# Kernel tuning notes

Hardware: AMD Instinct MI355X
Metric: run time of the kernel (lower is better)

The kernel has to match this reference:

```python
import jax, jax.numpy as jnp
import numpy as np

B, D, A, K, M = 32768, 64, 32, 16, 128


def _spec(W):
    # SpectralLinear: weight divided by its largest singular value
    s = jnp.linalg.norm(W, ord=2)
    return W / (s + 1e-6)


def setup_inputs() -> dict:
    key = jax.random.key(0)
    ks = jax.random.split(key, 20)

    def rn(i, shape):
        return jax.random.normal(ks[i], shape, jnp.float32) / np.float32(np.sqrt(shape[0]))

    return {
        "z": jax.random.normal(ks[0], (B, D), jnp.float32),
        "action": jax.random.normal(ks[1], (B, A), jnp.float32),
        "rw": jax.random.uniform(ks[2], (B, K), jnp.float32),
        "control": jax.random.normal(ks[3], (B, D), jnp.float32),
        # ActionTokenizer(action_dim, d_model, latent_dim) params (act / control / chart)
        "act_Wx": rn(4, (A + D, M)), "act_bx": jnp.zeros((M,), jnp.float32), "act_Wz": rn(5, (A, D)),
        "ctl_Wx": rn(6, (2 * D, M)), "ctl_bx": jnp.zeros((M,), jnp.float32), "ctl_Wz": rn(7, (D, D)),
        "cht_Wx": rn(8, (K + D, M)), "cht_bx": jnp.zeros((M,), jnp.float32), "cht_Wz": rn(9, (K, D)),
        # z_embed
        "We": rn(10, (D, M)), "be": jnp.zeros((M,), jnp.float32),
        # CovariantAttention (n_heads=1)
        "Wq": rn(11, (M, M)), "Wk": rn(12, (M, M)), "Wv": rn(13, (M, M)), "Wo": rn(14, (M, M)),
        # Spectral output heads
        "cons_W": rn(15, (M, 1)), "cons_b": jnp.zeros((1,), jnp.float32),
        "form_W": rn(16, (M, D)), "form_b": jnp.zeros((D,), jnp.float32),
    }


def reference(z, action, rw, control,
              act_Wx, act_bx, act_Wz,
              ctl_Wx, ctl_bx, ctl_Wz,
              cht_Wx, cht_bx, cht_Wz,
              We, be, Wq, Wk, Wv, Wo,
              cons_W, cons_b, form_W, form_b):
    def tok(u, Wx, bx, Wz):
        # tokenizer: feature token in d_model + associated latent position token
        x = jnp.tanh(jnp.concatenate([u, z], axis=-1) @ Wx + bx)   # [B, M]
        zt = z + jnp.tanh(u @ Wz)                                   # [B, D]
        return x, zt

    act_x, act_z = tok(action, act_Wx, act_bx, act_Wz)
    ctl_x, ctl_z = tok(control, ctl_Wx, ctl_bx, ctl_Wz)
    cht_x, cht_z = tok(rw, cht_Wx, cht_bx, cht_Wz)

    ctx_x = jnp.stack([act_x, ctl_x, cht_x], axis=1)  # [B, 3, M]
    ctx_z = jnp.stack([act_z, ctl_z, cht_z], axis=1)  # [B, 3, D]

    x_q = z @ We + be                                  # [B, M]

    # CovariantAttention: dot-product scores with metric-aware (geodesic distance) bias
    q = x_q @ Wq                                       # [B, M]
    k = ctx_x @ Wk                                     # [B, 3, M]
    v = ctx_x @ Wv                                     # [B, 3, M]
    dist2 = jnp.sum((z[:, None, :] - ctx_z) ** 2, axis=-1)          # [B, 3]
    scores = jnp.einsum('bm,btm->bt', q, k) / np.float32(np.sqrt(M)) - dist2
    attn = jax.nn.softmax(scores, axis=-1)             # [B, 3]
    feat = jnp.einsum('bt,btm->bm', attn, v) @ Wo      # [B, M]

    # Spectral output heads
    reward_conservative = feat @ _spec(cons_W) + cons_b            # [B, 1]
    reward_form_cov = feat @ _spec(form_W) + form_b                # [B, D]
    reward_nonconservative = jnp.sum(reward_form_cov * control, axis=-1, keepdims=True)

    return reward_conservative + reward_nonconservative            # [B, 1]
```

## Files before the change

### kernel.cpp

```cpp
#include <hip/hip_runtime.h>
#include <hip/hip_bf16.h>


typedef float f32x4 __attribute__((ext_vector_type(4)));
typedef short s16x8 __attribute__((ext_vector_type(8)));

#define OFF_ACTX  0
#define OFF_CTLX  24
#define OFF_CHTX  56
#define OFF_ACTZ  80
#define OFF_CTLZ  84
#define OFF_CHTZ  92
#define OFF_WEQK  96
#define OFF_WVOFT 112
#define N_TILES   128
#define SIG_OFF   (N_TILES*1024)
#define PREP_OFF  (SIG_OFF + 256)

__device__ __forceinline__ unsigned short f2bf(float f){
  unsigned u = __float_as_uint(f);
  u += 0x7fffu + ((u>>16)&1u);
  return (unsigned short)(u>>16);
}
__device__ __forceinline__ float ubf_lo(unsigned u){ return __uint_as_float(u<<16); }
__device__ __forceinline__ float ubf_hi(unsigned u){ return __uint_as_float(u & 0xffff0000u); }

union V8 { s16x8 v; unsigned short us[8]; uint4 q; };

__device__ __forceinline__ f32x4 MF(s16x8 a, s16x8 b, f32x4 c){
  return __builtin_amdgcn_mfma_f32_16x16x32_bf16(a, b, c, 0, 0, 0);
}

__device__ __forceinline__ s16x8 ldB(const unsigned short* pk, int tile, int lane){
  V8 t;
  t.q = *reinterpret_cast<const uint4*>(pk + ((tile<<6) + lane)*8);
  return t.v;
}

__device__ __forceinline__ s16x8 ldA_g(const float* __restrict__ p, int ko, int limit){
  V8 t;
  if (ko < limit){
    const float4* q4 = reinterpret_cast<const float4*>(p + ko);
    float4 a = q4[0], b = q4[1];
    t.us[0]=f2bf(a.x); t.us[1]=f2bf(a.y); t.us[2]=f2bf(a.z); t.us[3]=f2bf(a.w);
    t.us[4]=f2bf(b.x); t.us[5]=f2bf(b.y); t.us[6]=f2bf(b.z); t.us[7]=f2bf(b.w);
  } else {
    t.q = make_uint4(0u,0u,0u,0u);
  }
  return t.v;
}

__device__ __forceinline__ float tanh_fast(float x){
  x = fminf(15.f, fmaxf(-15.f, x));
  float e = __expf(2.f*x);
  return 1.f - __fdividef(2.f, e + 1.f);
}

__global__ __launch_bounds__(256) void prep_all(
    const float* __restrict__ We, const float* __restrict__ be,
    const float* __restrict__ Wq, const float* __restrict__ Wk,
    const float* __restrict__ Wv, const float* __restrict__ Wo,
    const float* __restrict__ consW, const float* __restrict__ formW,
    const float* __restrict__ aWx, const float* __restrict__ cWx,
    const float* __restrict__ hWx, const float* __restrict__ aWz,
    const float* __restrict__ cWz, const float* __restrict__ hWz,
    unsigned short* __restrict__ packed, float* __restrict__ prep,
    float* __restrict__ sig)
{
  const int b = blockIdx.x;
  const int tid = threadIdx.x;

  if (b < 130){
    __shared__ float Msh[128][129];
    __shared__ float tsh[128];
    if (b <= 64){
      for (int idx = tid; idx < 16384; idx += 256)
        Msh[idx >> 7][idx & 127] = Wk[idx];
      const float* rowv = (b == 64) ? be : (We + (size_t)b*128);
      if (tid < 128){
        float s = 0.f;
        for (int m = 0; m < 128; ++m) s += rowv[m]*Wq[(size_t)m*128 + tid];
        tsh[tid] = s;
      }
      __syncthreads();
      if (tid < 128){
        float s1 = 0.f;
        for (int p = 0; p < 128; ++p) s1 += tsh[p]*Msh[tid][p];
        if (b == 64) prep[16384 + tid] = s1;
        else {
          int r = b;
          int T = OFF_WEQK + ((r>>5)<<3) + (tid>>4);
          int l2 = (((r&31)>>3)<<4) | (tid&15);
          packed[((size_t)T*64 + l2)*8 + (r&7)] = f2bf(s1);
        }
      }
    } else {
      int d = b - 65;
      for (int idx = tid; idx < 16384; idx += 256)
        Msh[idx >> 7][idx & 127] = Wo[idx];
      __syncthreads();
      if (tid < 128){
        float s = 0.f;
        if (d < 64){ for (int j = 0; j < 128; ++j) s += Msh[tid][j]*formW[(size_t)j*64 + d]; }
        else       { for (int j = 0; j < 128; ++j) s += Msh[tid][j]*consW[j]; }
        tsh[tid] = s;
      }
      __syncthreads();
      for (int idx = tid; idx < 16384; idx += 256)
        Msh[idx >> 7][idx & 127] = Wv[idx];
      __syncthreads();
      if (tid < 128){
        float s1 = 0.f;
        for (int p = 0; p < 128; ++p) s1 += Msh[tid][p]*tsh[p];
        if (d < 64){
          int r = d;
          int T = OFF_WVOFT + ((r>>5)<<3) + (tid>>4);
          int l2 = (((r&31)>>3)<<4) | (tid&15);
          packed[((size_t)T*64 + l2)*8 + (r&7)] = f2bf(s1);
        } else prep[16512 + tid] = s1;
      }
    }
    return;
  }

  if (b == 130){
    __shared__ unsigned short SW[8192];
    __shared__ unsigned short SG[4096];

    #pragma unroll
    for (int s4 = 0; s4 < 4; ++s4){
      int q = tid*4 + s4;
      int T = q >> 6, l = q & 63;
      V8 t;
      #pragma unroll
      for (int i = 0; i < 8; ++i){
        int k = (T>>2)*32 + ((l>>4)<<3) + i;
        int n = ((T&3)<<4) + (l&15);
        t.us[i] = f2bf(formW[(size_t)k*64 + n]);
      }
      *reinterpret_cast<uint4*>(&SW[q*8]) = t.q;
    }
    __syncthreads();
    if (tid >= 64) return;
    const int l = tid;
    const f32x4 z4 = {0.f,0.f,0.f,0.f};

    float cs;
    { float c0 = consW[l], c1 = consW[l+64];
      cs = c0*c0 + c1*c1;
      #pragma unroll
      for (int m = 1; m < 64; m <<= 1) cs += __shfl_xor(cs, m);
    }

    s16x8 wf[4][4];
    #pragma unroll
    for (int kt = 0; kt < 4; ++kt)
      #pragma unroll
      for (int x = 0; x < 4; ++x)
        wf[kt][x] = *reinterpret_cast<const s16x8*>(&SW[((((kt<<2)+x)<<6) | l)*8]);

    f32x4 D[4][4];
    #pragma unroll
    for (int it = 0; it < 4; ++it)
      #pragma unroll
      for (int nt = 0; nt < 4; ++nt){
        f32x4 a = z4;
        #pragma unroll
        for (int kt = 0; kt < 4; ++kt) a = MF(wf[kt][it], wf[kt][nt], a);
        D[it][nt] = a;
      }

    float L;
    {
      float ss = 0.f;
      #pragma unroll
      for (int it = 0; it < 4; ++it)
        #pragma unroll
        for (int nt = 0; nt < 4; ++nt)
          #pragma unroll
          for (int j = 0; j < 4; ++j) ss += D[it][nt][j]*D[it][nt][j];
      #pragma unroll
      for (int m = 1; m < 64; m <<= 1) ss += __shfl_xor(ss, m);
      float n0 = sqrtf(ss);
      L = logf(n0);
      float iv = 1.f/n0;
      #pragma unroll
      for (int it = 0; it < 4; ++it){
        int rb  = it*16 + ((l>>4)<<2);
        int lp  = (((rb&31)>>3)<<4) | (l&15);
        int ib  = rb & 7;
        int ktg = rb >> 5;
        #pragma unroll
        for (int nt = 0; nt < 4; ++nt){
          unsigned w0 = (unsigned)f2bf(D[it][nt][0]*iv) | ((unsigned)f2bf(D[it][nt][1]*iv)<<16);
          unsigned w1 = (unsigned)f2bf(D[it][nt][2]*iv) | ((unsigned)f2bf(D[it][nt][3]*iv)<<16);
          uint2 u; u.x = w0; u.y = w1;
          *reinterpret_cast<uint2*>(&SG[((((ktg<<2)+nt)<<6 | lp))*8 + ib]) = u;
        }
      }
    }

    for (int s = 1; s <= 6; ++s){
      s16x8 gf[2][4];
      #pragma unroll
      for (int kt = 0; kt < 2; ++kt)
        #pragma unroll
        for (int x = 0; x < 4; ++x)
          gf[kt][x] = *reinterpret_cast<const s16x8*>(&SG[((((kt<<2)+x)<<6) | l)*8]);
      f32x4 E[4][4];
      #pragma unroll
      for (int it = 0; it < 4; ++it)
        #pragma unroll
        for (int nt = 0; nt < 4; ++nt){
          f32x4 a = MF(gf[0][it], gf[0][nt], z4);
          E[it][nt] = MF(gf[1][it], gf[1][nt], a);
        }
      float ss = 0.f;
      #pragma unroll
      for (int it = 0; it < 4; ++it)
        #pragma unroll
        for (int nt = 0; nt < 4; ++nt)
          #pragma unroll
          for (int j = 0; j < 4; ++j) ss += E[it][nt][j]*E[it][nt][j];
      #pragma unroll
      for (int m = 1; m < 64; m <<= 1) ss += __shfl_xor(ss, m);
      float ns = sqrtf(ss);
      L = 2.f*L + logf(ns);
      if (s < 6){
        float iv = 1.f/ns;
        #pragma unroll
        for (int it = 0; it < 4; ++it){
          int rb  = it*16 + ((l>>4)<<2);
          int lp  = (((rb&31)>>3)<<4) | (l&15);
          int ib  = rb & 7;
          int ktg = rb >> 5;
          #pragma unroll
          for (int nt = 0; nt < 4; ++nt){
            unsigned w0 = (unsigned)f2bf(E[it][nt][0]*iv) | ((unsigned)f2bf(E[it][nt][1]*iv)<<16);
            unsigned w1 = (unsigned)f2bf(E[it][nt][2]*iv) | ((unsigned)f2bf(E[it][nt][3]*iv)<<16);
            uint2 u; u.x = w0; u.y = w1;
            *reinterpret_cast<uint2*>(&SG[((((ktg<<2)+nt)<<6 | lp))*8 + ib]) = u;
          }
        }
      }
    }

    if (l == 0){
      float sf = expf(L*(1.f/128.f));
      sig[0] = 1.f/(sf + 1e-6f);
      sig[1] = 1.f/(sqrtf(cs) + 1e-6f);
    }
    return;
  }

  {
    int tile = b - 131;
    const float* W; int N; int kind = 0; int base;
    if      (tile < 24) { W=aWx; N=128; base=OFF_ACTX; }
    else if (tile < 56) { W=cWx; N=128; base=OFF_CTLX; }
    else if (tile < 80) { W=hWx; N=128; base=OFF_CHTX; kind=1; }
    else if (tile < 84) { W=aWz; N=64;  base=OFF_ACTZ; }
    else if (tile < 92) { W=cWz; N=64;  base=OFF_CTLZ; }
    else                { W=hWz; N=64;  base=OFF_CHTZ; kind=2; }
    int NT = N >> 4;
    int lt = tile - base;
    int nt = lt % NT, kt = lt / NT;
    int l = tid >> 2, i0 = (tid & 3)*2;
    unsigned short us2[2];
    #pragma unroll
    for (int di = 0; di < 2; ++di){
      int i = i0 + di;
      int k = kt*32 + ((l>>4)<<3) + i;
      int n = nt*16 + (l & 15);
      int sr = k;
      if (kind == 1) sr = (k < 16) ? k : (k < 32 ? -1 : k - 16);
      else if (kind == 2) sr = (k < 16) ? k : -1;
      float v = (sr >= 0) ? W[(size_t)sr*N + n] : 0.f;
      us2[di] = f2bf(v);
    }
    *reinterpret_cast<unsigned*>(&packed[((size_t)tile*64 + l)*8 + i0]) =
        (unsigned)us2[0] | ((unsigned)us2[1] << 16);
  }
}

template<int KTX, int KTZ>
__device__ __forceinline__ void token2(
    const unsigned short* pk, int offX, const s16x8 (*afX)[2],
    int offZ, const s16x8 (*afZ)[2], const float* __restrict__ bx,
    int lane, int ntb, int nzb, unsigned xp[2][4][2], float d2p[2][4])
{
  const int r15 = lane & 15;
  const f32x4 z4 = {0.f,0.f,0.f,0.f};
  f32x4 acc[2][4];
  #pragma unroll
  for (int s = 0; s < 2; ++s)
    #pragma unroll
    for (int nl = 0; nl < 4; ++nl) acc[s][nl] = z4;
  #pragma unroll
  for (int kt = 0; kt < KTX; ++kt){
    #pragma unroll
    for (int nl = 0; nl < 4; ++nl){
      s16x8 b = ldB(pk, offX + kt*8 + ntb + nl, lane);
      acc[0][nl] = MF(afX[kt][0], b, acc[0][nl]);
      acc[1][nl] = MF(afX[kt][1], b, acc[1][nl]);
    }
  }
  #pragma unroll
  for (int s = 0; s < 2; ++s)
    #pragma unroll
    for (int nl = 0; nl < 4; ++nl){
      float bv = bx[(ntb + nl)*16 + r15];
      float v0 = tanh_fast(acc[s][nl][0] + bv);
      float v1 = tanh_fast(acc[s][nl][1] + bv);
      float v2 = tanh_fast(acc[s][nl][2] + bv);
      float v3 = tanh_fast(acc[s][nl][3] + bv);
      xp[s][nl][0] = (unsigned)f2bf(v0) | ((unsigned)f2bf(v1) << 16);
      xp[s][nl][1] = (unsigned)f2bf(v2) | ((unsigned)f2bf(v3) << 16);
    }
  f32x4 a2[2][2];
  #pragma unroll
  for (int s = 0; s < 2; ++s)
    #pragma unroll
    for (int nl = 0; nl < 2; ++nl) a2[s][nl] = z4;
  #pragma unroll
  for (int kt = 0; kt < KTZ; ++kt){
    #pragma unroll
    for (int nl = 0; nl < 2; ++nl){
      s16x8 b = ldB(pk, offZ + kt*4 + nzb + nl, lane);
      a2[0][nl] = MF(afZ[kt][0], b, a2[0][nl]);
      a2[1][nl] = MF(afZ[kt][1], b, a2[1][nl]);
    }
  }
  #pragma unroll
  for (int s = 0; s < 2; ++s)
    #pragma unroll
    for (int j = 0; j < 4; ++j){
      float t0 = tanh_fast(a2[s][0][j]);
      float t1 = tanh_fast(a2[s][1][j]);
      d2p[s][j] = t0*t0 + t1*t1;
    }
}

__global__ __launch_bounds__(512, 2) void reward_main(
    const float* __restrict__ z, const float* __restrict__ action,
    const float* __restrict__ rw, const float* __restrict__ control,
    const float* __restrict__ act_bx, const float* __restrict__ ctl_bx,
    const float* __restrict__ cht_bx, const float* __restrict__ consb,
    const float* __restrict__ formb,
    const unsigned short* __restrict__ packed, const float* __restrict__ prep,
    const float* __restrict__ sig, float* __restrict__ out)
{
  __shared__ unsigned short pk_sh[65536];
  __shared__ float exS[4][2][2][3][16];
  __shared__ float exT[4][2][2][16];

  const int tid  = threadIdx.x;
  const int wid  = tid >> 6;
  const int lane = tid & 63;
  const int rg   = wid & 3;
  const int mh   = wid >> 2;
  const int g0   = blockIdx.x*128 + rg*32;
  const int r15  = lane & 15;
  const int hi   = lane >> 4;
  const int ko   = hi << 3;
  const int rb   = hi << 2;
  const int ntb  = mh << 2;
  const int nzb  = mh << 1;
  const f32x4 z4 = {0.f,0.f,0.f,0.f};

  s16x8 fz0[2], fz1[2], fac[2], fc0[2], fc1[2], frw[2];
  #pragma unroll
  for (int s = 0; s < 2; ++s){
    const int ar = g0 + s*16 + r15;
    fz0[s] = ldA_g(z + (size_t)ar*64,            ko, 64);
    fz1[s] = ldA_g(z + (size_t)ar*64 + 32,       ko, 32);
    fac[s] = ldA_g(action + (size_t)ar*32,       ko, 32);
    fc0[s] = ldA_g(control + (size_t)ar*64,      ko, 64);
    fc1[s] = ldA_g(control + (size_t)ar*64 + 32, ko, 32);
    frw[s] = ldA_g(rw + (size_t)ar*16,           ko, 16);
  }

  {
    uint4* d4 = reinterpret_cast<uint4*>(pk_sh);
    const uint4* s4 = reinterpret_cast<const uint4*>(packed);
    #pragma unroll
    for (int it = 0; it < 16; ++it)
      d4[it*512 + tid] = s4[it*512 + tid];
  }
  __syncthreads();
  const unsigned short* pk = pk_sh;

  unsigned xpk[3][2][4][2];
  float d2[3][2][4];
  {
    s16x8 afA[3][2] = {{fac[0],fac[1]},{fz0[0],fz0[1]},{fz1[0],fz1[1]}};
    s16x8 afAz[1][2] = {{fac[0],fac[1]}};
    token2<3,1>(pk, OFF_ACTX, afA, OFF_ACTZ, afAz, act_bx, lane, ntb, nzb, xpk[0], d2[0]);
  }
  {
    s16x8 afC[4][2] = {{fc0[0],fc0[1]},{fc1[0],fc1[1]},{fz0[0],fz0[1]},{fz1[0],fz1[1]}};
    s16x8 afCz[2][2] = {{fc0[0],fc0[1]},{fc1[0],fc1[1]}};
    token2<4,2>(pk, OFF_CTLX, afC, OFF_CTLZ, afCz, ctl_bx, lane, ntb, nzb, xpk[1], d2[1]);
  }
  {
    s16x8 afH[3][2] = {{frw[0],frw[1]},{fz0[0],fz0[1]},{fz1[0],fz1[1]}};
    s16x8 afHz[1][2] = {{frw[0],frw[1]}};
    token2<3,1>(pk, OFF_CHTX, afH, OFF_CHTZ, afHz, cht_bx, lane, ntb, nzb, xpk[2], d2[2]);
  }

  f32x4 qw[2][4];
  {
    #pragma unroll
    for (int s = 0; s < 2; ++s)
      #pragma unroll
      for (int nl = 0; nl < 4; ++nl) qw[s][nl] = z4;
    #pragma unroll
    for (int kt = 0; kt < 2; ++kt){
      #pragma unroll
      for (int nl = 0; nl < 4; ++nl){
        s16x8 b = ldB(pk, OFF_WEQK + kt*8 + ntb + nl, lane);
        qw[0][nl] = MF(kt == 0 ? fz0[0] : fz1[0], b, qw[0][nl]);
        qw[1][nl] = MF(kt == 0 ? fz0[1] : fz1[1], b, qw[1][nl]);
      }
    }
    const float* bqk = prep + 16384;
    #pragma unroll
    for (int nl = 0; nl < 4; ++nl){
      float bv = bqk[(ntb + nl)*16 + r15];
      #pragma unroll
      for (int s = 0; s < 2; ++s)
        #pragma unroll
        for (int j = 0; j < 4; ++j) qw[s][nl][j] += bv;
    }
  }

  const float isq = 0.0883883476483184f;
  float scp[2][3][4];
  #pragma unroll
  for (int s = 0; s < 2; ++s)
    #pragma unroll
    for (int t = 0; t < 3; ++t){
      float p0s = 0.f, p1s = 0.f, p2s = 0.f, p3s = 0.f;
      #pragma unroll
      for (int nl = 0; nl < 4; ++nl){
        unsigned p0 = xpk[t][s][nl][0], p1 = xpk[t][s][nl][1];
        p0s += ubf_lo(p0)*qw[s][nl][0];
        p1s += ubf_hi(p0)*qw[s][nl][1];
        p2s += ubf_lo(p1)*qw[s][nl][2];
        p3s += ubf_hi(p1)*qw[s][nl][3];
      }
      scp[s][t][0] = p0s*isq - d2[t][s][0];
      scp[s][t][1] = p1s*isq - d2[t][s][1];
      scp[s][t][2] = p2s*isq - d2[t][s][2];
      scp[s][t][3] = p3s*isq - d2[t][s][3];
    }
  #pragma unroll
  for (int m = 1; m < 16; m <<= 1)
    #pragma unroll
    for (int s = 0; s < 2; ++s)
      #pragma unroll
      for (int t = 0; t < 3; ++t)
        #pragma unroll
        for (int j = 0; j < 4; ++j) scp[s][t][j] += __shfl_xor(scp[s][t][j], m);

  if (r15 == 0){
    #pragma unroll
    for (int s = 0; s < 2; ++s)
      #pragma unroll
      for (int t = 0; t < 3; ++t)
        #pragma unroll
        for (int j = 0; j < 4; ++j) exS[rg][mh][s][t][rb+j] = scp[s][t][j];
  }
  __syncthreads();

  float at[2][3][4];
  #pragma unroll
  for (int s = 0; s < 2; ++s)
    #pragma unroll
    for (int j = 0; j < 4; ++j){
      int r = rb + j;
      float s0 = exS[rg][0][s][0][r] + exS[rg][1][s][0][r];
      float s1 = exS[rg][0][s][1][r] + exS[rg][1][s][1][r];
      float s2 = exS[rg][0][s][2][r] + exS[rg][1][s][2][r];
      float mx = fmaxf(s0, fmaxf(s1, s2));
      float e0 = __expf(s0 - mx), e1 = __expf(s1 - mx), e2 = __expf(s2 - mx);
      float inv = 1.f/(e0 + e1 + e2);
      at[s][0][j] = e0*inv; at[s][1][j] = e1*inv; at[s][2][j] = e2*inv;
    }

  float xb[2][4][4];
  #pragma unroll
  for (int s = 0; s < 2; ++s)
    #pragma unroll
    for (int nl = 0; nl < 4; ++nl)
      #pragma unroll
      for (int j = 0; j < 4; ++j){
        unsigned p = xpk[0][s][nl][j>>1];
        float v = at[s][0][j] * ((j&1) ? ubf_hi(p) : ubf_lo(p));
        p = xpk[1][s][nl][j>>1];
        v += at[s][1][j] * ((j&1) ? ubf_hi(p) : ubf_lo(p));
        p = xpk[2][s][nl][j>>1];
        v += at[s][2][j] * ((j&1) ? ubf_hi(p) : ubf_lo(p));
        xb[s][nl][j] = v;
      }

  f32x4 g[2][4];
  {
    #pragma unroll
    for (int s = 0; s < 2; ++s)
      #pragma unroll
      for (int nl = 0; nl < 4; ++nl) g[s][nl] = z4;
    #pragma unroll
    for (int kt = 0; kt < 2; ++kt){
      #pragma unroll
      for (int nl = 0; nl < 4; ++nl){
        s16x8 b = ldB(pk, OFF_WVOFT + kt*8 + ntb + nl, lane);
        g[0][nl] = MF(kt == 0 ? fc0[0] : fc1[0], b, g[0][nl]);
        g[1][nl] = MF(kt == 0 ? fc0[1] : fc1[1], b, g[1][nl]);
      }
    }
  }

  const float inv_f = sig[0], inv_c = sig[1], cb = consb[0];
  const float* wvoc = prep + 16512;
  float wv[4];
  #pragma unroll
  for (int nl = 0; nl < 4; ++nl) wv[nl] = wvoc[(ntb + nl)*16 + r15];

  float tot[2][4];
  #pragma unroll
  for (int s = 0; s < 2; ++s)
    #pragma unroll
    for (int j = 0; j < 4; ++j){
      float sc = 0.f, sg = 0.f;
      #pragma unroll
      for (int nl = 0; nl < 4; ++nl){
        sc += xb[s][nl][j]*wv[nl];
        sg += xb[s][nl][j]*g[s][nl][j];
      }
      tot[s][j] = inv_c*sc + inv_f*sg;
    }
  #pragma unroll
  for (int m = 1; m < 16; m <<= 1)
    #pragma unroll
    for (int s = 0; s < 2; ++s)
      #pragma unroll
      for (int j = 0; j < 4; ++j) tot[s][j] += __shfl_xor(tot[s][j], m);

  if (r15 == 0){
    #pragma unroll
    for (int s = 0; s < 2; ++s)
      #pragma unroll
      for (int j = 0; j < 4; ++j) exT[rg][mh][s][rb+j] = tot[s][j];
  }
  __syncthreads();

  if (mh == 0){
    #pragma unroll
    for (int s = 0; s < 2; ++s){
      const int ar = g0 + s*16 + r15;
      float fbp;
      {
        const float* cp = control + (size_t)ar*64;
        float4 c0a = *(const float4*)(cp + ko);
        float4 c0b = *(const float4*)(cp + ko + 4);
        float4 c1a = *(const float4*)(cp + 32 + ko);
        float4 c1b = *(const float4*)(cp + 32 + ko + 4);
        float4 f0a = *(const float4*)(formb + ko);
        float4 f0b = *(const float4*)(formb + ko + 4);
        float4 f1a = *(const float4*)(formb + 32 + ko);
        float4 f1b = *(const float4*)(formb + 32 + ko + 4);
        fbp = c0a.x*f0a.x + c0a.y*f0a.y + c0a.z*f0a.z + c0a.w*f0a.w
            + c0b.x*f0b.x + c0b.y*f0b.y + c0b.z*f0b.z + c0b.w*f0b.w
            + c1a.x*f1a.x + c1a.y*f1a.y + c1a.z*f1a.z + c1a.w*f1a.w
            + c1b.x*f1b.x + c1b.y*f1b.y + c1b.z*f1b.z + c1b.w*f1b.w;
      }
      fbp += __shfl_xor(fbp, 16);
      fbp += __shfl_xor(fbp, 32);
      float fbj[4];
      #pragma unroll
      for (int j = 0; j < 4; ++j) fbj[j] = __shfl(fbp, hi*4 + j);
      if (r15 == 0){
        #pragma unroll
        for (int j = 0; j < 4; ++j){
          int r = rb + j;
          out[g0 + s*16 + r] = exT[rg][0][s][r] + exT[rg][1][s][r] + fbj[j] + cb;
        }
      }
    }
  }
}

extern "C" void kernel_launch(void* const* d_in, const int* in_sizes, int n_in,
                              void* d_out, int out_size, void* d_ws, size_t ws_size,
                              hipStream_t stream)
{
  const float* z      = (const float*)d_in[0];
  const float* action = (const float*)d_in[1];
  const float* rw     = (const float*)d_in[2];
  const float* control= (const float*)d_in[3];
  const float* actWx  = (const float*)d_in[4];
  const float* actbx  = (const float*)d_in[5];
  const float* actWz  = (const float*)d_in[6];
  const float* ctlWx  = (const float*)d_in[7];
  const float* ctlbx  = (const float*)d_in[8];
  const float* ctlWz  = (const float*)d_in[9];
  const float* chtWx  = (const float*)d_in[10];
  const float* chtbx  = (const float*)d_in[11];
  const float* chtWz  = (const float*)d_in[12];
  const float* We     = (const float*)d_in[13];
  const float* be     = (const float*)d_in[14];
  const float* Wq     = (const float*)d_in[15];
  const float* Wk     = (const float*)d_in[16];
  const float* Wv     = (const float*)d_in[17];
  const float* Wo     = (const float*)d_in[18];
  const float* consW  = (const float*)d_in[19];
  const float* consb  = (const float*)d_in[20];
  const float* formW  = (const float*)d_in[21];
  const float* formb  = (const float*)d_in[22];
  float* out = (float*)d_out;

  unsigned short* packed = (unsigned short*)d_ws;
  float* sig  = (float*)((char*)d_ws + SIG_OFF);
  float* prep = (float*)((char*)d_ws + PREP_OFF);

  hipLaunchKernelGGL(prep_all, dim3(227), dim3(256), 0, stream,
                     We, be, Wq, Wk, Wv, Wo, consW, formW,
                     actWx, ctlWx, chtWx, actWz, ctlWz, chtWz,
                     packed, prep, sig);
  hipLaunchKernelGGL(reward_main, dim3(256), dim3(512), 0, stream,
                     z, action, rw, control, actbx, ctlbx, chtbx,
                     consb, formb, packed, prep, sig, out);
}
```

Measured before the change: 38.87 us.

## Fold attention output head into per-token dot products and restructure reduction

Computes the combined Wv·Wo·head vector per row up front, so each token contributes only scalar score and head-projection dots. This drops storage of the bf16 token features and the second weighted-sum pass. Partial sums are reduced through a padded shared array and a single thread per row does the softmax and output. Other changes: async global-to-LDS loads for the packed weights, packed bf16 conversion instructions, rcp-based tanh without clamping, and a parallelised prep kernel. The unclamped tanh could hit overflow edge cases, although exp to inf still gives the right sign.

```diff
diff --git a/kernel.cpp b/kernel.cpp
--- a/kernel.cpp
+++ b/kernel.cpp
@@ -22,8 +22,12 @@
   u += 0x7fffu + ((u>>16)&1u);
   return (unsigned short)(u>>16);
 }
-__device__ __forceinline__ float ubf_lo(unsigned u){ return __uint_as_float(u<<16); }
-__device__ __forceinline__ float ubf_hi(unsigned u){ return __uint_as_float(u & 0xffff0000u); }
+
+__device__ __forceinline__ unsigned cvtpk(float lo, float hi){
+  unsigned r;
+  asm("v_cvt_pk_bf16_f32 %0, %1, %2" : "=v"(r) : "v"(lo), "v"(hi));
+  return r;
+}
 
 union V8 { s16x8 v; unsigned short us[8]; uint4 q; };
 
@@ -42,8 +46,7 @@
   if (ko < limit){
     const float4* q4 = reinterpret_cast<const float4*>(p + ko);
     float4 a = q4[0], b = q4[1];
-    t.us[0]=f2bf(a.x); t.us[1]=f2bf(a.y); t.us[2]=f2bf(a.z); t.us[3]=f2bf(a.w);
-    t.us[4]=f2bf(b.x); t.us[5]=f2bf(b.y); t.us[6]=f2bf(b.z); t.us[7]=f2bf(b.w);
+    t.q = make_uint4(cvtpk(a.x,a.y), cvtpk(a.z,a.w), cvtpk(b.x,b.y), cvtpk(b.z,b.w));
   } else {
     t.q = make_uint4(0u,0u,0u,0u);
   }
@@ -51,9 +54,8 @@
 }
 
 __device__ __forceinline__ float tanh_fast(float x){
-  x = fminf(15.f, fmaxf(-15.f, x));
   float e = __expf(2.f*x);
-  return 1.f - __fdividef(2.f, e + 1.f);
+  return 1.f - 2.f*__builtin_amdgcn_rcpf(e + 1.f);
 }
 
 __global__ __launch_bounds__(256) void prep_all(
@@ -73,19 +75,32 @@
   if (b < 130){
     __shared__ float Msh[128][129];
     __shared__ float tsh[128];
+    __shared__ float ph[2][128];
+    const int half = tid >> 7, t128 = tid & 127;
+    const int m0 = half*64;
     if (b <= 64){
-      for (int idx = tid; idx < 16384; idx += 256)
-        Msh[idx >> 7][idx & 127] = Wk[idx];
+      for (int i4 = tid; i4 < 4096; i4 += 256){
+        float4 v = ((const float4*)Wk)[i4];
+        int r = i4 >> 5, c = (i4 & 31) << 2;
+        Msh[r][c] = v.x; Msh[r][c+1] = v.y; Msh[r][c+2] = v.z; Msh[r][c+3] = v.w;
+      }
       const float* rowv = (b == 64) ? be : (We + (size_t)b*128);
+      {
+        float s = 0.f;
+        for (int m = m0; m < m0+64; ++m) s += rowv[m]*Wq[(size_t)m*128 + t128];
+        ph[half][t128] = s;
+      }
+      __syncthreads();
+      if (tid < 128) tsh[tid] = ph[0][tid] + ph[1][tid];
+      __syncthreads();
+      {
+        float s1 = 0.f;
+        for (int p = m0; p < m0+64; ++p) s1 += tsh[p]*Msh[t128][p];
+        ph[half][t128] = s1;
+      }
+      __syncthreads();
       if (tid < 128){
-        float s = 0.f;
-        for (int m = 0; m < 128; ++m) s += rowv[m]*Wq[(size_t)m*128 + tid];
-        tsh[tid] = s;
-      }
-      __syncthreads();
-      if (tid < 128){
-        float s1 = 0.f;
-        for (int p = 0; p < 128; ++p) s1 += tsh[p]*Msh[tid][p];
+        float s1 = ph[0][tid] + ph[1][tid];
         if (b == 64) prep[16384 + tid] = s1;
         else {
           int r = b;
@@ -96,22 +111,35 @@
       }
     } else {
       int d = b - 65;
-      for (int idx = tid; idx < 16384; idx += 256)
-        Msh[idx >> 7][idx & 127] = Wo[idx];
+      for (int i4 = tid; i4 < 4096; i4 += 256){
+        float4 v = ((const float4*)Wo)[i4];
+        int r = i4 >> 5, c = (i4 & 31) << 2;
+        Msh[r][c] = v.x; Msh[r][c+1] = v.y; Msh[r][c+2] = v.z; Msh[r][c+3] = v.w;
+      }
+      __syncthreads();
+      {
+        float s = 0.f;
+        if (d < 64){ for (int j = m0; j < m0+64; ++j) s += Msh[t128][j]*formW[(size_t)j*64 + d]; }
+        else       { for (int j = m0; j < m0+64; ++j) s += Msh[t128][j]*consW[j]; }
+        ph[half][t128] = s;
+      }
+      __syncthreads();
+      if (tid < 128) tsh[tid] = ph[0][tid] + ph[1][tid];
+      __syncthreads();
+      for (int i4 = tid; i4 < 4096; i4 += 256){
+        float4 v = ((const float4*)Wv)[i4];
+        int r = i4 >> 5, c = (i4 & 31) << 2;
+        Msh[r][c] = v.x; Msh[r][c+1] = v.y; Msh[r][c+2] = v.z; Msh[r][c+3] = v.w;
+      }
+      __syncthreads();
+      {
+        float s1 = 0.f;
+        for (int p = m0; p < m0+64; ++p) s1 += Msh[t128][p]*tsh[p];
+        ph[half][t128] = s1;
+      }
       __syncthreads();
       if (tid < 128){
-        float s = 0.f;
-        if (d < 64){ for (int j = 0; j < 128; ++j) s += Msh[tid][j]*formW[(size_t)j*64 + d]; }
-        else       { for (int j = 0; j < 128; ++j) s += Msh[tid][j]*consW[j]; }
-        tsh[tid] = s;
-      }
-      __syncthreads();
-      for (int idx = tid; idx < 16384; idx += 256)
-        Msh[idx >> 7][idx & 127] = Wv[idx];
-      __syncthreads();
-      if (tid < 128){
-        float s1 = 0.f;
-        for (int p = 0; p < 128; ++p) s1 += Msh[tid][p]*tsh[p];
+        float s1 = ph[0][tid] + ph[1][tid];
         if (d < 64){
           int r = d;
           int T = OFF_WVOFT + ((r>>5)<<3) + (tid>>4);
@@ -284,10 +312,12 @@
 }
 
 template<int KTX, int KTZ>
-__device__ __forceinline__ void token2(
+__device__ __forceinline__ void token_dot2(
     const unsigned short* pk, int offX, const s16x8 (*afX)[2],
     int offZ, const s16x8 (*afZ)[2], const float* __restrict__ bx,
-    int lane, int ntb, int nzb, unsigned xp[2][4][2], float d2p[2][4])
+    int lane, int ntb, int nzb,
+    const f32x4 qw[2][4], const f32x4 hw[2][4],
+    float st[2][4], float hs[2][4])
 {
   const int r15 = lane & 15;
   const f32x4 z4 = {0.f,0.f,0.f,0.f};
@@ -300,44 +330,49 @@
   for (int kt = 0; kt < KTX; ++kt){
     #pragma unroll
     for (int nl = 0; nl < 4; ++nl){
-      s16x8 b = ldB(pk, offX + kt*8 + ntb + nl, lane);
-      acc[0][nl] = MF(afX[kt][0], b, acc[0][nl]);
-      acc[1][nl] = MF(afX[kt][1], b, acc[1][nl]);
-    }
-  }
+      s16x8 bfr = ldB(pk, offX + kt*8 + ntb + nl, lane);
+      acc[0][nl] = MF(afX[kt][0], bfr, acc[0][nl]);
+      acc[1][nl] = MF(afX[kt][1], bfr, acc[1][nl]);
+    }
+  }
+  float qs[2][4], hp[2][4];
   #pragma unroll
   for (int s = 0; s < 2; ++s)
     #pragma unroll
-    for (int nl = 0; nl < 4; ++nl){
-      float bv = bx[(ntb + nl)*16 + r15];
-      float v0 = tanh_fast(acc[s][nl][0] + bv);
-      float v1 = tanh_fast(acc[s][nl][1] + bv);
-      float v2 = tanh_fast(acc[s][nl][2] + bv);
-      float v3 = tanh_fast(acc[s][nl][3] + bv);
-      xp[s][nl][0] = (unsigned)f2bf(v0) | ((unsigned)f2bf(v1) << 16);
-      xp[s][nl][1] = (unsigned)f2bf(v2) | ((unsigned)f2bf(v3) << 16);
-    }
+    for (int j = 0; j < 4; ++j){ qs[s][j] = 0.f; hp[s][j] = 0.f; }
+  #pragma unroll
+  for (int nl = 0; nl < 4; ++nl){
+    float bv = bx[(ntb + nl)*16 + r15];
+    #pragma unroll
+    for (int s = 0; s < 2; ++s)
+      #pragma unroll
+      for (int j = 0; j < 4; ++j){
+        float x = tanh_fast(acc[s][nl][j] + bv);
+        qs[s][j] += x*qw[s][nl][j];
+        hp[s][j] += x*hw[s][nl][j];
+      }
+  }
   f32x4 a2[2][2];
   #pragma unroll
-  for (int s = 0; s < 2; ++s)
-    #pragma unroll
-    for (int nl = 0; nl < 2; ++nl) a2[s][nl] = z4;
+  for (int s = 0; s < 2; ++s){ a2[s][0] = z4; a2[s][1] = z4; }
   #pragma unroll
   for (int kt = 0; kt < KTZ; ++kt){
     #pragma unroll
     for (int nl = 0; nl < 2; ++nl){
-      s16x8 b = ldB(pk, offZ + kt*4 + nzb + nl, lane);
-      a2[0][nl] = MF(afZ[kt][0], b, a2[0][nl]);
-      a2[1][nl] = MF(afZ[kt][1], b, a2[1][nl]);
-    }
-  }
+      s16x8 bfr = ldB(pk, offZ + kt*4 + nzb + nl, lane);
+      a2[0][nl] = MF(afZ[kt][0], bfr, a2[0][nl]);
+      a2[1][nl] = MF(afZ[kt][1], bfr, a2[1][nl]);
+    }
+  }
+  const float isq = 0.0883883476483184f;
   #pragma unroll
   for (int s = 0; s < 2; ++s)
     #pragma unroll
     for (int j = 0; j < 4; ++j){
       float t0 = tanh_fast(a2[s][0][j]);
       float t1 = tanh_fast(a2[s][1][j]);
-      d2p[s][j] = t0*t0 + t1*t1;
+      st[s][j] = qs[s][j]*isq - (t0*t0 + t1*t1);
+      hs[s][j] = hp[s][j];
     }
 }
 
@@ -351,8 +386,7 @@
     const float* __restrict__ sig, float* __restrict__ out)
 {
   __shared__ unsigned short pk_sh[65536];
-  __shared__ float exS[4][2][2][3][16];
-  __shared__ float exT[4][2][2][16];
+  __shared__ float ex[128][49];
 
   const int tid  = threadIdx.x;
   const int wid  = tid >> 6;
@@ -368,6 +402,19 @@
   const int nzb  = mh << 1;
   const f32x4 z4 = {0.f,0.f,0.f,0.f};
 
+  {
+    auto* gsrc = (const __attribute__((address_space(1))) char*)packed;
+    auto* ldst = (__attribute__((address_space(3))) char*)pk_sh;
+    #pragma unroll
+    for (int it = 0; it < 16; ++it){
+      int off = it*8192 + wid*1024;
+      __builtin_amdgcn_global_load_lds(
+        (const __attribute__((address_space(1))) unsigned*)(gsrc + off + lane*16),
+        (__attribute__((address_space(3))) unsigned*)(ldst + off),
+        16, 0, 0);
+    }
+  }
+
   s16x8 fz0[2], fz1[2], fac[2], fc0[2], fc1[2], frw[2];
   #pragma unroll
   for (int s = 0; s < 2; ++s){
@@ -380,214 +427,147 @@
     frw[s] = ldA_g(rw + (size_t)ar*16,           ko, 16);
   }
 
-  {
-    uint4* d4 = reinterpret_cast<uint4*>(pk_sh);
-    const uint4* s4 = reinterpret_cast<const uint4*>(packed);
-    #pragma unroll
-    for (int it = 0; it < 16; ++it)
-      d4[it*512 + tid] = s4[it*512 + tid];
-  }
+  if (mh == 0){
+    #pragma unroll
+    for (int s = 0; s < 2; ++s){
+      const int ar = g0 + s*16 + r15;
+      const float* cp = control + (size_t)ar*64;
+      float4 c0a = *(const float4*)(cp + ko);
+      float4 c0b = *(const float4*)(cp + ko + 4);
+      float4 c1a = *(const float4*)(cp + 32 + ko);
+      float4 c1b = *(const float4*)(cp + 32 + ko + 4);
+      float4 f0a = *(const float4*)(formb + ko);
+      float4 f0b = *(const float4*)(formb + ko + 4);
+      float4 f1a = *(const float4*)(formb + 32 + ko);
+      float4 f1b = *(const float4*)(formb + 32 + ko + 4);
+      float fbp = c0a.x*f0a.x + c0a.y*f0a.y + c0a.z*f0a.z + c0a.w*f0a.w
+                + c0b.x*f0b.x + c0b.y*f0b.y + c0b.z*f0b.z + c0b.w*f0b.w
+                + c1a.x*f1a.x + c1a.y*f1a.y + c1a.z*f1a.z + c1a.w*f1a.w
+                + c1b.x*f1b.x + c1b.y*f1b.y + c1b.z*f1b.z + c1b.w*f1b.w;
+      fbp += __shfl_xor(fbp, 16);
+      fbp += __shfl_xor(fbp, 32);
+      if (lane < 16) ex[rg*32 + s*16 + r15][48] = fbp;
+    }
+  }
+
+  const float inv_f = sig[0], inv_c = sig[1];
+
   __syncthreads();
   const unsigned short* pk = pk_sh;
 
-  unsigned xpk[3][2][4][2];
-  float d2[3][2][4];
+  f32x4 qw[2][4];
+  {
+    #pragma unroll
+    for (int s = 0; s < 2; ++s)
+      #pragma unroll
+      for (int nl = 0; nl < 4; ++nl) qw[s][nl] = z4;
+    #pragma unroll
+    for (int kt = 0; kt < 2; ++kt){
+      #pragma unroll
+      for (int nl = 0; nl < 4; ++nl){
+        s16x8 bfr = ldB(pk, OFF_WEQK + kt*8 + ntb + nl, lane);
+        qw[0][nl] = MF(kt == 0 ? fz0[0] : fz1[0], bfr, qw[0][nl]);
+        qw[1][nl] = MF(kt == 0 ? fz0[1] : fz1[1], bfr, qw[1][nl]);
+      }
+    }
+    const float* bqk = prep + 16384;
+    #pragma unroll
+    for (int nl = 0; nl < 4; ++nl){
+      float bv = bqk[(ntb + nl)*16 + r15];
+      #pragma unroll
+      for (int s = 0; s < 2; ++s)
+        #pragma unroll
+        for (int j = 0; j < 4; ++j) qw[s][nl][j] += bv;
+    }
+  }
+
+  f32x4 hw[2][4];
+  {
+    #pragma unroll
+    for (int s = 0; s < 2; ++s)
+      #pragma unroll
+      for (int nl = 0; nl < 4; ++nl) hw[s][nl] = z4;
+    #pragma unroll
+    for (int kt = 0; kt < 2; ++kt){
+      #pragma unroll
+      for (int nl = 0; nl < 4; ++nl){
+        s16x8 bfr = ldB(pk, OFF_WVOFT + kt*8 + ntb + nl, lane);
+        hw[0][nl] = MF(kt == 0 ? fc0[0] : fc1[0], bfr, hw[0][nl]);
+        hw[1][nl] = MF(kt == 0 ? fc0[1] : fc1[1], bfr, hw[1][nl]);
+      }
+    }
+    const float* wvoc = prep + 16512;
+    #pragma unroll
+    for (int nl = 0; nl < 4; ++nl){
+      float wvc = inv_c*wvoc[(ntb + nl)*16 + r15];
+      #pragma unroll
+      for (int s = 0; s < 2; ++s)
+        #pragma unroll
+        for (int j = 0; j < 4; ++j) hw[s][nl][j] = wvc + inv_f*hw[s][nl][j];
+    }
+  }
+
+  float st[3][2][4], hs[3][2][4];
   {
     s16x8 afA[3][2] = {{fac[0],fac[1]},{fz0[0],fz0[1]},{fz1[0],fz1[1]}};
     s16x8 afAz[1][2] = {{fac[0],fac[1]}};
-    token2<3,1>(pk, OFF_ACTX, afA, OFF_ACTZ, afAz, act_bx, lane, ntb, nzb, xpk[0], d2[0]);
+    token_dot2<3,1>(pk, OFF_ACTX, afA, OFF_ACTZ, afAz, act_bx, lane, ntb, nzb, qw, hw, st[0], hs[0]);
   }
   {
     s16x8 afC[4][2] = {{fc0[0],fc0[1]},{fc1[0],fc1[1]},{fz0[0],fz0[1]},{fz1[0],fz1[1]}};
     s16x8 afCz[2][2] = {{fc0[0],fc0[1]},{fc1[0],fc1[1]}};
-    token2<4,2>(pk, OFF_CTLX, afC, OFF_CTLZ, afCz, ctl_bx, lane, ntb, nzb, xpk[1], d2[1]);
+    token_dot2<4,2>(pk, OFF_CTLX, afC, OFF_CTLZ, afCz, ctl_bx, lane, ntb, nzb, qw, hw, st[1], hs[1]);
   }
   {
     s16x8 afH[3][2] = {{frw[0],frw[1]},{fz0[0],fz0[1]},{fz1[0],fz1[1]}};
     s16x8 afHz[1][2] = {{frw[0],frw[1]}};
-    token2<3,1>(pk, OFF_CHTX, afH, OFF_CHTZ, afHz, cht_bx, lane, ntb, nzb, xpk[2], d2[2]);
-  }
-
-  f32x4 qw[2][4];
-  {
+    token_dot2<3,1>(pk, OFF_CHTX, afH, OFF_CHTZ, afHz, cht_bx, lane, ntb, nzb, qw, hw, st[2], hs[2]);
+  }
+
+  #pragma unroll
+  for (int m = 1; m < 4; m <<= 1)
+    #pragma unroll
+    for (int t = 0; t < 3; ++t)
+      #pragma unroll
+      for (int s = 0; s < 2; ++s)
+        #pragma unroll
+        for (int j = 0; j < 4; ++j){
+          st[t][s][j] += __shfl_xor(st[t][s][j], m);
+          hs[t][s][j] += __shfl_xor(hs[t][s][j], m);
+        }
+  if ((r15 & 3) == 0){
+    int gi = r15 >> 2;
     #pragma unroll
     for (int s = 0; s < 2; ++s)
       #pragma unroll
-      for (int nl = 0; nl < 4; ++nl) qw[s][nl] = z4;
-    #pragma unroll
-    for (int kt = 0; kt < 2; ++kt){
-      #pragma unroll
-      for (int nl = 0; nl < 4; ++nl){
-        s16x8 b = ldB(pk, OFF_WEQK + kt*8 + ntb + nl, lane);
-        qw[0][nl] = MF(kt == 0 ? fz0[0] : fz1[0], b, qw[0][nl]);
-        qw[1][nl] = MF(kt == 0 ? fz0[1] : fz1[1], b, qw[1][nl]);
-      }
-    }
-    const float* bqk = prep + 16384;
-    #pragma unroll
-    for (int nl = 0; nl < 4; ++nl){
-      float bv = bqk[(ntb + nl)*16 + r15];
-      #pragma unroll
-      for (int s = 0; s < 2; ++s)
-        #pragma unroll
-        for (int j = 0; j < 4; ++j) qw[s][nl][j] += bv;
-    }
-  }
-
-  const float isq = 0.0883883476483184f;
-  float scp[2][3][4];
-  #pragma unroll
-  for (int s = 0; s < 2; ++s)
+      for (int t = 0; t < 3; ++t)
+        #pragma unroll
+        for (int j = 0; j < 4; ++j){
+          int row = rg*32 + s*16 + rb + j;
+          ex[row][t*8 + mh*4 + gi]      = st[t][s][j];
+          ex[row][24 + t*8 + mh*4 + gi] = hs[t][s][j];
+        }
+  }
+  __syncthreads();
+
+  if (tid < 128){
+    const int row = tid;
+    float sv[3], hv[3];
     #pragma unroll
     for (int t = 0; t < 3; ++t){
-      float p0s = 0.f, p1s = 0.f, p2s = 0.f, p3s = 0.f;
-      #pragma unroll
-      for (int nl = 0; nl < 4; ++nl){
-        unsigned p0 = xpk[t][s][nl][0], p1 = xpk[t][s][nl][1];
-        p0s += ubf_lo(p0)*qw[s][nl][0];
-        p1s += ubf_hi(p0)*qw[s][nl][1];
-        p2s += ubf_lo(p1)*qw[s][nl][2];
-        p3s += ubf_hi(p1)*qw[s][nl][3];
-      }
-      scp[s][t][0] = p0s*isq - d2[t][s][0];
-      scp[s][t][1] = p1s*isq - d2[t][s][1];
-      scp[s][t][2] = p2s*isq - d2[t][s][2];
-      scp[s][t][3] = p3s*isq - d2[t][s][3];
-    }
-  #pragma unroll
-  for (int m = 1; m < 16; m <<= 1)
-    #pragma unroll
-    for (int s = 0; s < 2; ++s)
-      #pragma unroll
-      for (int t = 0; t < 3; ++t)
-        #pragma unroll
-        for (int j = 0; j < 4; ++j) scp[s][t][j] += __shfl_xor(scp[s][t][j], m);
-
-  if (r15 == 0){
-    #pragma unroll
-    for (int s = 0; s < 2; ++s)
-      #pragma unroll
-      for (int t = 0; t < 3; ++t)
-        #pragma unroll
-        for (int j = 0; j < 4; ++j) exS[rg][mh][s][t][rb+j] = scp[s][t][j];
-  }
-  __syncthreads();
-
-  float at[2][3][4];
-  #pragma unroll
-  for (int s = 0; s < 2; ++s)
-    #pragma unroll
-    for (int j = 0; j < 4; ++j){
-      int r = rb + j;
-      float s0 = exS[rg][0][s][0][r] + exS[rg][1][s][0][r];
-      float s1 = exS[rg][0][s][1][r] + exS[rg][1][s][1][r];
-      float s2 = exS[rg][0][s][2][r] + exS[rg][1][s][2][r];
-      float mx = fmaxf(s0, fmaxf(s1, s2));
-      float e0 = __expf(s0 - mx), e1 = __expf(s1 - mx), e2 = __expf(s2 - mx);
-      float inv = 1.f/(e0 + e1 + e2);
-      at[s][0][j] = e0*inv; at[s][1][j] = e1*inv; at[s][2][j] = e2*inv;
-    }
-
-  float xb[2][4][4];
-  #pragma unroll
-  for (int s = 0; s < 2; ++s)
-    #pragma unroll
-    for (int nl = 0; nl < 4; ++nl)
-      #pragma unroll
-      for (int j = 0; j < 4; ++j){
-        unsigned p = xpk[0][s][nl][j>>1];
-        float v = at[s][0][j] * ((j&1) ? ubf_hi(p) : ubf_lo(p));
-        p = xpk[1][s][nl][j>>1];
-        v += at[s][1][j] * ((j&1) ? ubf_hi(p) : ubf_lo(p));
-        p = xpk[2][s][nl][j>>1];
-        v += at[s][2][j] * ((j&1) ? ubf_hi(p) : ubf_lo(p));
-        xb[s][nl][j] = v;
-      }
-
-  f32x4 g[2][4];
-  {
-    #pragma unroll
-    for (int s = 0; s < 2; ++s)
-      #pragma unroll
-      for (int nl = 0; nl < 4; ++nl) g[s][nl] = z4;
-    #pragma unroll
-    for (int kt = 0; kt < 2; ++kt){
-      #pragma unroll
-      for (int nl = 0; nl < 4; ++nl){
-        s16x8 b = ldB(pk, OFF_WVOFT + kt*8 + ntb + nl, lane);
-        g[0][nl] = MF(kt == 0 ? fc0[0] : fc1[0], b, g[0][nl]);
-        g[1][nl] = MF(kt == 0 ? fc0[1] : fc1[1], b, g[1][nl]);
-      }
-    }
-  }
-
-  const float inv_f = sig[0], inv_c = sig[1], cb = consb[0];
-  const float* wvoc = prep + 16512;
-  float wv[4];
-  #pragma unroll
-  for (int nl = 0; nl < 4; ++nl) wv[nl] = wvoc[(ntb + nl)*16 + r15];
-
-  float tot[2][4];
-  #pragma unroll
-  for (int s = 0; s < 2; ++s)
-    #pragma unroll
-    for (int j = 0; j < 4; ++j){
-      float sc = 0.f, sg = 0.f;
-      #pragma unroll
-      for (int nl = 0; nl < 4; ++nl){
-        sc += xb[s][nl][j]*wv[nl];
-        sg += xb[s][nl][j]*g[s][nl][j];
-      }
-      tot[s][j] = inv_c*sc + inv_f*sg;
-    }
-  #pragma unroll
-  for (int m = 1; m < 16; m <<= 1)
-    #pragma unroll
-    for (int s = 0; s < 2; ++s)
-      #pragma unroll
-      for (int j = 0; j < 4; ++j) tot[s][j] += __shfl_xor(tot[s][j], m);
-
-  if (r15 == 0){
-    #pragma unroll
-    for (int s = 0; s < 2; ++s)
-      #pragma unroll
-      for (int j = 0; j < 4; ++j) exT[rg][mh][s][rb+j] = tot[s][j];
-  }
-  __syncthreads();
-
-  if (mh == 0){
-    #pragma unroll
-    for (int s = 0; s < 2; ++s){
-      const int ar = g0 + s*16 + r15;
-      float fbp;
-      {
-        const float* cp = control + (size_t)ar*64;
-        float4 c0a = *(const float4*)(cp + ko);
-        float4 c0b = *(const float4*)(cp + ko + 4);
-        float4 c1a = *(const float4*)(cp + 32 + ko);
-        float4 c1b = *(const float4*)(cp + 32 + ko + 4);
-        float4 f0a = *(const float4*)(formb + ko);
-        float4 f0b = *(const float4*)(formb + ko + 4);
-        float4 f1a = *(const float4*)(formb + 32 + ko);
-        float4 f1b = *(const float4*)(formb + 32 + ko + 4);
-        fbp = c0a.x*f0a.x + c0a.y*f0a.y + c0a.z*f0a.z + c0a.w*f0a.w
-            + c0b.x*f0b.x + c0b.y*f0b.y + c0b.z*f0b.z + c0b.w*f0b.w
-            + c1a.x*f1a.x + c1a.y*f1a.y + c1a.z*f1a.z + c1a.w*f1a.w
-            + c1b.x*f1b.x + c1b.y*f1b.y + c1b.z*f1b.z + c1b.w*f1b.w;
-      }
-      fbp += __shfl_xor(fbp, 16);
-      fbp += __shfl_xor(fbp, 32);
-      float fbj[4];
-      #pragma unroll
-      for (int j = 0; j < 4; ++j) fbj[j] = __shfl(fbp, hi*4 + j);
-      if (r15 == 0){
-        #pragma unroll
-        for (int j = 0; j < 4; ++j){
-          int r = rb + j;
-          out[g0 + s*16 + r] = exT[rg][0][s][r] + exT[rg][1][s][r] + fbj[j] + cb;
-        }
-      }
-    }
+      float a = 0.f, h = 0.f;
+      #pragma unroll
+      for (int i = 0; i < 8; ++i){
+        a += ex[row][t*8 + i];
+        h += ex[row][24 + t*8 + i];
+      }
+      sv[t] = a; hv[t] = h;
+    }
+    float mx = fmaxf(sv[0], fmaxf(sv[1], sv[2]));
+    float e0 = __expf(sv[0]-mx), e1 = __expf(sv[1]-mx), e2 = __expf(sv[2]-mx);
+    float inv = __builtin_amdgcn_rcpf(e0 + e1 + e2);
+    float tot = (e0*hv[0] + e1*hv[1] + e2*hv[2])*inv + ex[row][48] + consb[0];
+    out[blockIdx.x*128 + row] = tot;
   }
 }
 
```

After: 33.06 us. -14.9%, faster.
